# Optimization experiments

Measured on AMD Instinct MI355X. Metric: run time of the kernel, lower is better.

Reference implementation:

```python
import jax, jax.numpy as jnp
import numpy as np

I_SIZE = 8      # interval_size
WS = 8          # window_size
SHIFT = 4       # window_size // 2
HG = 4          # grid-attn heads (num_heads // 2)
HS = 4          # swin/window heads (num_heads // 2)


def cln(x, g, b, eps=1e-5):
    # channel LayerNorm over axis 1 of NCHW
    mu = x.mean(axis=1, keepdims=True)
    var = ((x - mu) ** 2).mean(axis=1, keepdims=True)
    return (x - mu) / jnp.sqrt(var + eps) * g[None, :, None, None] + b[None, :, None, None]


def conv1x1(x, w, b):
    return jnp.einsum('bchw,oc->bohw', x, w) + b[None, :, None, None]


def grid_shuffle(x, I):
    B, C, H, W = x.shape
    H1, W1 = H // I, W // I
    x = x.reshape(B, C, H1, I, W1, I).transpose(0, 3, 5, 1, 2, 4)
    return x.reshape(B * I * I, C, H1, W1)


def grid_unshuffle(x, I):
    Bi, C, H1, W1 = x.shape
    B = Bi // (I * I)
    x = x.reshape(B, I, I, C, H1, W1).transpose(0, 3, 4, 1, 5, 2)
    return x.reshape(B, C, H1 * I, W1 * I)


def rel_pos_index(wh, ww):
    coords = np.stack(np.meshgrid(np.arange(wh), np.arange(ww), indexing='ij')).reshape(2, -1)
    rel = (coords[:, :, None] - coords[:, None, :]).transpose(1, 2, 0)
    rel[:, :, 0] += wh - 1
    rel[:, :, 1] += ww - 1
    rel[:, :, 0] *= 2 * ww - 1
    return rel.sum(-1)  # (N, N) int


def dyn_pos_bias(H1, W1, w1, b1, w2, b2, w3, b3):
    # dynamic position bias MLP: (2,) relative coords -> heads
    ch = np.arange(1 - H1, H1, dtype=np.float32)
    cw = np.arange(1 - W1, W1, dtype=np.float32)
    rel = np.stack(np.meshgrid(ch, cw, indexing='ij'), axis=-1).reshape(-1, 2)
    t = jnp.asarray(rel)
    t = jax.nn.relu(t @ w1.T + b1)
    t = jax.nn.relu(t @ w2.T + b2)
    t = t @ w3.T + b3  # ((2H1-1)*(2W1-1), heads)
    idx = rel_pos_index(H1, W1)
    return t[idx].transpose(2, 0, 1)[None]  # (1, heads, N, N)


def mha2d(q, k, v, bias, heads, pw, pb):
    B, C, H, W = q.shape
    hd, N = C // heads, H * W
    sp = lambda t: t.reshape(B, heads, hd, N).transpose(0, 1, 3, 2)
    qh, kh, vh = sp(q), sp(k), sp(v)
    attn = jax.nn.softmax(jnp.einsum('bhnd,bhmd->bhnm', qh * hd ** -0.5, kh) + bias, axis=-1)
    out = jnp.einsum('bhnm,bhmd->bhnd', attn, vh).transpose(0, 1, 3, 2).reshape(B, C, H, W)
    return conv1x1(out, pw, pb)


def swin_mask(H, W, ws, shift):
    img = np.zeros((H, W), np.float32)
    cnt = 0
    for hs in (slice(0, H - ws), slice(H - ws, H - shift), slice(H - shift, H)):
        for wsl in (slice(0, W - ws), slice(W - ws, W - shift), slice(W - shift, W)):
            img[hs, wsl] = cnt
            cnt += 1
    mw = img.reshape(H // ws, ws, W // ws, ws).transpose(0, 2, 1, 3).reshape(-1, ws * ws)
    m = mw[:, None, :] - mw[:, :, None]
    return jnp.asarray(np.where(m != 0, -100.0, 0.0).astype(np.float32))  # (nW, N, N)


def swin_attn(x, qkv_w, qkv_b, rpb, pw, pb, ws, shift, heads):
    B, C, H, W = x.shape
    hd, N = C // heads, ws * ws
    if shift > 0:
        x = jnp.roll(x, (-shift, -shift), axis=(2, 3))
    nh, nw = H // ws, W // ws
    nW = nh * nw
    xw = x.reshape(B, C, nh, ws, nw, ws).transpose(0, 2, 4, 3, 5, 1).reshape(B * nW, N, C)
    qkv = (xw @ qkv_w.T + qkv_b).reshape(B * nW, N, 3, heads, hd).transpose(2, 0, 3, 1, 4)
    q, k, v = qkv[0], qkv[1], qkv[2]
    attn = jnp.einsum('bhnd,bhmd->bhnm', q * hd ** -0.5, k)
    attn = attn + rpb[rel_pos_index(ws, ws)].transpose(2, 0, 1)[None]
    if shift > 0:
        mask = swin_mask(H, W, ws, shift)
        attn = (attn.reshape(B, nW, heads, N, N) + mask[None, :, None]).reshape(B * nW, heads, N, N)
    attn = jax.nn.softmax(attn, axis=-1)
    out = jnp.einsum('bhnm,bhmd->bhnd', attn, v).transpose(0, 2, 1, 3).reshape(B * nW, N, C)
    out = out @ pw.T + pb
    out = out.reshape(B, nh, nw, ws, ws, C).transpose(0, 5, 1, 3, 2, 4).reshape(B, C, H, W)
    if shift > 0:
        out = jnp.roll(out, (shift, shift), axis=(2, 3))
    return out


def setup_inputs() -> dict:
    ks = iter(jax.random.split(jax.random.key(0), 64))
    w = lambda *s: jax.random.normal(next(ks), s, jnp.float32) * 0.02
    d, dg, ds, hid = 128, 64, 32, 256
    return dict(
        x=jax.random.normal(next(ks), (4, d, 128, 128), jnp.float32),
        ln_g=jnp.ones(d), ln_b=jnp.zeros(d),
        ga_qkv_w=w(3 * dg, dg), ga_qkv_b=jnp.zeros(3 * dg),
        ga_gp_w=w(dg, dg), ga_gp_b=jnp.zeros(dg),
        pos_w1=w(16, 2), pos_b1=jnp.zeros(16),
        pos_w2=w(16, 16), pos_b2=jnp.zeros(16),
        pos_w3=w(HG, 16), pos_b3=jnp.zeros(HG),
        a1_pw=w(dg, dg), a1_pb=jnp.zeros(dg),
        a2_pw=w(dg, dg), a2_pb=jnp.zeros(dg),
        sw_qkv_w=w(3 * ds, ds), sw_qkv_b=jnp.zeros(3 * ds),
        sw_rpb=w((2 * WS - 1) ** 2, HS), sw_pw=w(ds, ds), sw_pb=jnp.zeros(ds),
        wn_qkv_w=w(3 * ds, ds), wn_qkv_b=jnp.zeros(3 * ds),
        wn_rpb=w((2 * WS - 1) ** 2, HS), wn_pw=w(ds, ds), wn_pb=jnp.zeros(ds),
        fc_w=w(d, d), fc_b=jnp.zeros(d),
        n2_g=jnp.ones(d), n2_b=jnp.zeros(d),
        m1_w=w(hid, d), m1_b=jnp.zeros(hid),
        m2_w=w(d, hid), m2_b=jnp.zeros(d),
    )


def reference(x, ln_g, ln_b, ga_qkv_w, ga_qkv_b, ga_gp_w, ga_gp_b,
              pos_w1, pos_b1, pos_w2, pos_b2, pos_w3, pos_b3,
              a1_pw, a1_pb, a2_pw, a2_pb,
              sw_qkv_w, sw_qkv_b, sw_rpb, sw_pw, sw_pb,
              wn_qkv_w, wn_qkv_b, wn_rpb, wn_pw, wn_pb,
              fc_w, fc_b, n2_g, n2_b, m1_w, m1_b, m2_w, m2_b):
    B, C, H, W = x.shape
    shortcut = x
    xg, xs, xw = jnp.split(x, [C // 2, C // 2 + C // 4], axis=1)

    # --- grid attention branch (C/2 channels) ---
    qkv = conv1x1(xg, ga_qkv_w, ga_qkv_b)
    x_grid = conv1x1(grid_shuffle(xg, I_SIZE), ga_gp_w, ga_gp_b)
    qkv = grid_shuffle(qkv, I_SIZE)
    H1, W1 = H // I_SIZE, W // I_SIZE
    pbias = dyn_pos_bias(H1, W1, pos_w1, pos_b1, pos_w2, pos_b2, pos_w3, pos_b3)
    q, k, v = jnp.split(qkv, 3, axis=1)
    t = mha2d(x_grid, k, v, pbias, HG, a1_pw, a1_pb)
    t = mha2d(q, x_grid, t, pbias, HG, a2_pw, a2_pb)
    xg_attn = grid_unshuffle(t, I_SIZE)

    # --- shifted / plain window attention branches (C/4 each) ---
    xs_attn = swin_attn(xs, sw_qkv_w, sw_qkv_b, sw_rpb, sw_pw, sw_pb, WS, SHIFT, HS)
    xw_attn = swin_attn(xw, wn_qkv_w, wn_qkv_b, wn_rpb, wn_pw, wn_pb, WS, 0, HS)

    x = jnp.concatenate([xw_attn, xs_attn, xg_attn], axis=1)
    x = cln(conv1x1(x, fc_w, fc_b), ln_g, ln_b)
    x = shortcut + x
    h = conv1x1(x, m1_w, m1_b)
    h = jax.nn.gelu(h, approximate=False)
    h = conv1x1(h, m2_w, m2_b)
    return x + cln(h, n2_g, n2_b) + shortcut
```

## Files before the change

### kernel.cpp

```cpp
#include <hip/hip_runtime.h>
#include <hip/hip_bf16.h>
#include <cstdint>


typedef __attribute__((ext_vector_type(8))) short bf8_t;
typedef __attribute__((ext_vector_type(4))) float f4_t;

__device__ __forceinline__ float bf2f(unsigned short u) {
  union { unsigned int i; float f; } x; x.i = ((unsigned int)u) << 16; return x.f;
}
__device__ __forceinline__ unsigned short f2bf(float f) {
  union { float f; unsigned int i; } x; x.f = f;
  unsigned int r = x.i + 0x7FFFu + ((x.i >> 16) & 1u);
  return (unsigned short)(r >> 16);
}
__device__ __forceinline__ unsigned int pk2(float a, float b) {
  unsigned int d;
  asm("v_cvt_pk_bf16_f32 %0, %1, %2" : "=v"(d) : "v"(a), "v"(b));
  return d;
}

#define MB (1048576L)

__global__ void pos_mlp_k(const float* __restrict__ w1, const float* __restrict__ b1,
                          const float* __restrict__ w2, const float* __restrict__ b2,
                          const float* __restrict__ w3, const float* __restrict__ b3,
                          float* __restrict__ table) {
  int j = blockIdx.x * 256 + threadIdx.x;
  if (j >= 961) return;
  float chv = (float)(j / 31) - 15.0f;
  float cwv = (float)(j % 31) - 15.0f;
  float t1[16], t2[16];
#pragma unroll
  for (int i = 0; i < 16; ++i) {
    float s = fmaf(w1[i * 2], chv, fmaf(w1[i * 2 + 1], cwv, b1[i]));
    t1[i] = fmaxf(s, 0.0f);
  }
#pragma unroll
  for (int i = 0; i < 16; ++i) {
    float s = b2[i];
#pragma unroll
    for (int k = 0; k < 16; ++k) s = fmaf(w2[i * 16 + k], t1[k], s);
    t2[i] = fmaxf(s, 0.0f);
  }
#pragma unroll
  for (int hh = 0; hh < 4; ++hh) {
    float s = b3[hh];
#pragma unroll
    for (int k = 0; k < 16; ++k) s = fmaf(w3[hh * 16 + k], t2[k], s);
    table[j * 4 + hh] = s;
  }
}

__global__ void pbT_gather_k(const float* __restrict__ table, float* __restrict__ pbT) {
  int t = blockIdx.x * 256 + threadIdx.x;
  int hh = t >> 16;
  int r = t & 65535;
  int m = r >> 8;
  int q = r & 255;
  int idx = ((q >> 4) - (m >> 4) + 15) * 31 + ((q & 15) - (m & 15) + 15);
  pbT[t] = table[idx * 4 + hh];
}

__global__ void rpbT_k(const float* __restrict__ rpb, float* __restrict__ rpbT) {
  int t = blockIdx.x * 256 + threadIdx.x;
  int h = t >> 12, r = t & 4095, m = r >> 6, n = r & 63;
  int idx = ((n >> 3) - (m >> 3) + 7) * 15 + ((n & 7) - (m & 7) + 7);
  rpbT[t] = rpb[idx * 4 + h];
}

__global__ void wq2_k(const float* __restrict__ sw_w, const float* __restrict__ sw_b,
                      const float* __restrict__ wn_w, const float* __restrict__ wn_b,
                      unsigned short* __restrict__ w2, float* __restrict__ b2) {
  const float QS = 0.35355339059327373f;
  int t = blockIdx.x * 256 + threadIdx.x;
  if (t < 12288) {
    int row = t >> 6, col = t & 63;
    float v = 0.0f;
    if (row < 96) { if (col < 32) v = sw_w[row * 32 + col]; }
    else          { if (col >= 32) v = wn_w[(row - 96) * 32 + col - 32]; }
    int rb = row % 96;
    if (rb < 32) v *= QS;
    w2[t] = f2bf(v);
  }
  if (t < 192) {
    float v = t < 96 ? sw_b[t] : wn_b[t - 96];
    if ((t % 96) < 32) v *= QS;
    b2[t] = v;
  }
}

__global__ void wcvt_k(const float* __restrict__ w0, const float* __restrict__ w1,
                       const float* __restrict__ w2, const float* __restrict__ w3,
                       const float* __restrict__ w4, const float* __restrict__ w5,
                       const float* __restrict__ w6,
                       const float* __restrict__ qkv_b, const float* __restrict__ gp_b,
                       unsigned short* __restrict__ dst, float* __restrict__ biasQG) {
  int t = blockIdx.x * 256 + threadIdx.x;
  if (t < 256) biasQG[t] = t < 192 ? qkv_b[t] : gp_b[t - 192] * 0.25f;
  if (t >= 106496) return;
  const float* src; int off; float sc = 1.0f;
  if (t < 12288)      { src = w0; off = 0; }
  else if (t < 16384) { src = w1; off = 12288; sc = 0.25f; }
  else if (t < 20480) { src = w2; off = 16384; }
  else if (t < 24576) { src = w3; off = 20480; }
  else if (t < 40960) { src = w4; off = 24576; }
  else if (t < 73728) { src = w5; off = 40960; }
  else                { src = w6; off = 73728; }
  dst[t] = f2bf(src[t - off] * sc);
}

__global__ __launch_bounds__(256) void tin_k(const float* __restrict__ x,
                                             unsigned short* __restrict__ xTb) {
  __shared__ float tile[64][132];
  const int b = blockIdx.z, px0 = blockIdx.x * 64, tid = threadIdx.x;
#pragma unroll
  for (int i = 0; i < 8; ++i) {
    int e = i * 256 + tid;
    int c = e >> 4, p4 = (e & 15) * 4;
    float4 v = *(const float4*)(x + (((size_t)(b * 128 + c)) << 14) + px0 + p4);
    tile[p4][c] = v.x; tile[p4 + 1][c] = v.y; tile[p4 + 2][c] = v.z; tile[p4 + 3][c] = v.w;
  }
  __syncthreads();
#pragma unroll
  for (int i = 0; i < 8; ++i) {
    int e = i * 256 + tid;
    int px = e >> 5, c4 = (e & 31) * 4;
    uint2 w = {pk2(tile[px][c4], tile[px][c4 + 1]), pk2(tile[px][c4 + 2], tile[px][c4 + 3])};
    *(uint2*)(xTb + ((size_t)(b * 16384 + px0 + px)) * 128 + c4) = w;
  }
}

template <int NF, int KC, int EPI, int OSHUF>
__global__ __launch_bounds__(256) void gemm_k(
    const unsigned short* __restrict__ A, int a_rs, int a_c0,
    const unsigned short* __restrict__ W, const float* __restrict__ bias,
    const float* __restrict__ g, const float* __restrict__ bb,
    const unsigned short* __restrict__ resf, const unsigned short* __restrict__ resb,
    void* __restrict__ out, int o_rs, int o_c0) {
  __shared__ __align__(16) char Asw[128 * 128];
  __shared__ __align__(16) char Bsw[NF * 16 * 128];
  const int tid = threadIdx.x;
  const int lane = tid & 63, wv = tid >> 6, wpx = wv * 32;
  const int lr = lane & 15, lg = lane >> 4;
  const int px0 = blockIdx.x * 128;
  const int co0 = blockIdx.y * (NF * 16);

  f4_t acc[2][NF];
#pragma unroll
  for (int mf = 0; mf < 2; ++mf)
#pragma unroll
    for (int nf = 0; nf < NF; ++nf) acc[mf][nf] = (f4_t){0.f, 0.f, 0.f, 0.f};

  for (int kc = 0; kc < KC; ++kc) {
    const int k0 = kc * 64;
    if (kc) __syncthreads();
#pragma unroll
    for (int i = 0; i < 4; ++i) {
      int e = i * 256 + tid;
      int row = e >> 3, q8 = e & 7;
      const unsigned short* src = A + (size_t)(px0 + row) * a_rs + a_c0 + k0 + q8 * 8;
      *(uint4*)(Asw + row * 128 + ((q8 ^ (row & 7)) << 4)) = *(const uint4*)src;
    }
#pragma unroll
    for (int i = 0; i < NF / 2; ++i) {
      int e = i * 256 + tid;
      int row = e >> 3, q8 = e & 7;
      const unsigned short* src = W + (size_t)(co0 + row) * (KC * 64) + k0 + q8 * 8;
      *(uint4*)(Bsw + row * 128 + ((q8 ^ (row & 7)) << 4)) = *(const uint4*)src;
    }
    __syncthreads();
#pragma unroll
    for (int ks = 0; ks < 2; ++ks) {
      const int xk = (((ks * 4) + lg) ^ (lane & 7)) << 4;
      bf8_t av[2], bv[NF];
#pragma unroll
      for (int mf = 0; mf < 2; ++mf)
        av[mf] = *(const bf8_t*)(Asw + (wpx + mf * 16 + lr) * 128 + xk);
#pragma unroll
      for (int nf = 0; nf < NF; ++nf)
        bv[nf] = *(const bf8_t*)(Bsw + (nf * 16 + lr) * 128 + xk);
#pragma unroll
      for (int mf = 0; mf < 2; ++mf)
#pragma unroll
        for (int nf = 0; nf < NF; ++nf)
          acc[mf][nf] = __builtin_amdgcn_mfma_f32_16x16x32_bf16(av[mf], bv[nf], acc[mf][nf], 0, 0, 0);
    }
  }

  float bco[NF];
#pragma unroll
  for (int nf = 0; nf < NF; ++nf) bco[nf] = bias[co0 + nf * 16 + lr];

  if constexpr (EPI >= 2) {
    float gv[NF], bbv[NF];
#pragma unroll
    for (int nf = 0; nf < NF; ++nf) { gv[nf] = g[nf * 16 + lr]; bbv[nf] = bb[nf * 16 + lr]; }
#pragma unroll
    for (int mf = 0; mf < 2; ++mf)
#pragma unroll
      for (int nf = 0; nf < NF; ++nf)
#pragma unroll
        for (int r = 0; r < 4; ++r) acc[mf][nf][r] += bco[nf];
#pragma unroll
    for (int mf = 0; mf < 2; ++mf) {
      float mus[4], rss[4];
#pragma unroll
      for (int r = 0; r < 4; ++r) {
        float s = 0.f, q = 0.f;
#pragma unroll
        for (int nf = 0; nf < NF; ++nf) {
          float v = acc[mf][nf][r];
          s += v; q += v * v;
        }
#pragma unroll
        for (int msk = 1; msk < 16; msk <<= 1) {
          s += __shfl_xor(s, msk);
          q += __shfl_xor(q, msk);
        }
        float mu = s * (1.0f / 128.0f);
        float var = q * (1.0f / 128.0f) - mu * mu;
        mus[r] = mu;
        rss[r] = rsqrtf(var + 1e-5f);
      }
      if constexpr (EPI == 2) {
#pragma unroll
        for (int r = 0; r < 4; ++r) {
          int px_e = px0 + wpx + mf * 16 + lg * 4 + r;
          const unsigned short* xr = resf + (size_t)px_e * 128 + lr;
          unsigned short* op = (unsigned short*)out + (size_t)px_e * o_rs + lr;
#pragma unroll
          for (int nf = 0; nf < NF; ++nf) {
            float v = (acc[mf][nf][r] - mus[r]) * rss[r] * gv[nf] + bbv[nf] + bf2f(xr[nf * 16]);
            op[nf * 16] = f2bf(v);
          }
        }
      } else {
        int pxb = px0 + wpx + mf * 16 + lg * 4;
        int b_ = pxb >> 14, p_ = pxb & 16383;
#pragma unroll
        for (int nf = 0; nf < NF; ++nf) {
          int ch = lr + nf * 16;
          float vr[4];
#pragma unroll
          for (int r = 0; r < 4; ++r) {
            float xv  = bf2f(resf[(size_t)(pxb + r) * 128 + ch]);
            float x2v = bf2f(resb[(size_t)(pxb + r) * 128 + ch]);
            vr[r] = (acc[mf][nf][r] - mus[r]) * rss[r] * gv[nf] + bbv[nf] + xv + x2v;
          }
          float4 v4 = {vr[0], vr[1], vr[2], vr[3]};
          *(float4*)((float*)out + (((size_t)(b_ * 128 + ch)) << 14) + p_) = v4;
        }
      }
    }
  } else {
#pragma unroll
    for (int mf = 0; mf < 2; ++mf) {
#pragma unroll
      for (int r = 0; r < 4; ++r) {
        int px_e = px0 + wpx + mf * 16 + lg * 4 + r;
        size_t orow;
        int cadj = co0;
        if constexpr (OSHUF == 0) {
          orow = (size_t)px_e;
        } else if constexpr (OSHUF == 1) {
          int b = px_e >> 14, p = px_e & 16383, hh = p >> 7, w_ = p & 127;
          orow = (size_t)(b * 64 + (hh & 7) * 8 + (w_ & 7)) * 256 + ((hh >> 3) * 16 + (w_ >> 3));
        } else if constexpr (OSHUF == 2) {
          int gbb = px_e >> 8, n = px_e & 255;
          int b = gbb >> 6, ih = (gbb >> 3) & 7, iw = gbb & 7;
          orow = (size_t)b * 16384 + ((n >> 4) * 8 + ih) * 128 + (n & 15) * 8 + iw;
        } else {
          int brx = (co0 >= 96);
          int b = px_e >> 14, p = px_e & 16383, hh = p >> 7, w_ = p & 127;
          int sh = brx ? 0 : 4;
          int h2 = (hh - sh) & 127, w2_ = (w_ - sh) & 127;
          orow = (size_t)brx * 65536 + (size_t)b * 16384 +
                 (size_t)(((h2 >> 3) * 16 + (w2_ >> 3)) * 64 + (h2 & 7) * 8 + (w2_ & 7));
          cadj = co0 - brx * 96;
        }
        unsigned short* op = (unsigned short*)out + orow * o_rs + o_c0 + cadj + lr;
#pragma unroll
        for (int nf = 0; nf < NF; ++nf) {
          float v = acc[mf][nf][r] + bco[nf];
          if constexpr (EPI == 1) v = 0.5f * v * (1.0f + erff(v * 0.7071067811865475f));
          op[nf * 16] = f2bf(v);
        }
      }
    }
  }
}

__global__ __launch_bounds__(256) void gattn_k(
    const unsigned short* __restrict__ Q, int q_rs, int q_c0,
    const unsigned short* __restrict__ K, int k_rs, int k_c0,
    const unsigned short* __restrict__ V, int v_rs, int v_c0,
    const float* __restrict__ pbT, unsigned short* __restrict__ outb, int o_rs, int o_c0) {
  __shared__ __align__(16) unsigned short K_lds[256 * 16];
  __shared__ __align__(16) unsigned short Vt[16 * 256];
  __shared__ __align__(16) unsigned short P_lds[4 * 64 * 32];
  const int gb = blockIdx.x, h = blockIdx.y, tid = threadIdx.x;
  const int lane = tid & 63, wv = tid >> 6;
  const int lr = lane & 15, lg = lane >> 4;
  const int q0 = wv * 64;

  {
    const unsigned short* kp = K + (size_t)(gb * 256 + tid) * k_rs + k_c0 + h * 16;
    *(uint4*)&K_lds[tid * 16]     = *(const uint4*)kp;
    *(uint4*)&K_lds[tid * 16 + 8] = *(const uint4*)(kp + 8);
    const unsigned short* vp = V + (size_t)(gb * 256 + tid) * v_rs + v_c0 + h * 16;
    uint4 va = *(const uint4*)vp;
    uint4 vb = *(const uint4*)(vp + 8);
    unsigned int w8[8] = {va.x, va.y, va.z, va.w, vb.x, vb.y, vb.z, vb.w};
    int chb = (tid >> 3);
    int wi = tid & 7;
#pragma unroll
    for (int w = 0; w < 8; ++w) {
      int d0 = 2 * w, d1 = 2 * w + 1;
      Vt[d0 * 256 + ((chb ^ (d0 & 7)) << 3) + wi] = (unsigned short)(w8[w] & 0xffff);
      Vt[d1 * 256 + ((chb ^ (d1 & 7)) << 3) + wi] = (unsigned short)(w8[w] >> 16);
    }
  }
  bf8_t bq[4];
  const bf8_t bz = {0, 0, 0, 0, 0, 0, 0, 0};
#pragma unroll
  for (int qt = 0; qt < 4; ++qt) {
    bq[qt] = bz;
    if (lg < 2)
      bq[qt] = *(const bf8_t*)(Q + (size_t)(gb * 256 + q0 + qt * 16 + lr) * q_rs + q_c0 + h * 16 + lg * 8);
  }
  __syncthreads();

  const f4_t z4 = {0.f, 0.f, 0.f, 0.f};
  f4_t oacc[4];
  float lrun[4];
#pragma unroll
  for (int qt = 0; qt < 4; ++qt) { oacc[qt] = z4; lrun[qt] = 0.0f; }

  unsigned short* Pw = &P_lds[wv * 64 * 32];

  for (int m0 = 0; m0 < 256; m0 += 32) {
    bf8_t ak0 = bz, ak1 = bz;
    if (lg < 2) {
      ak0 = *(const bf8_t*)&K_lds[(m0 + lr) * 16 + lg * 8];
      ak1 = *(const bf8_t*)&K_lds[(m0 + 16 + lr) * 16 + lg * 8];
    }
    bf8_t av = *(const bf8_t*)&Vt[lr * 256 + ((((m0 >> 3) + lg) ^ (lr & 7)) << 3)];

#pragma unroll
    for (int qt = 0; qt < 4; ++qt) {
      const float* bpm = pbT + ((size_t)(h * 256 + m0 + lg * 4) << 8) + q0 + qt * 16 + lr;
      f4_t c0v = {bpm[0], bpm[256], bpm[512], bpm[768]};
      f4_t c1v = {bpm[4096], bpm[4352], bpm[4608], bpm[4864]};
      f4_t st0 = __builtin_amdgcn_mfma_f32_16x16x32_bf16(ak0, bq[qt], c0v, 0, 0, 0);
      f4_t st1 = __builtin_amdgcn_mfma_f32_16x16x32_bf16(ak1, bq[qt], c1v, 0, 0, 0);
      float p0[4], p1[4], ls = 0.0f;
#pragma unroll
      for (int r = 0; r < 4; ++r) {
        p0[r] = __expf(st0[r]);
        p1[r] = __expf(st1[r]);
        ls += p0[r] + p1[r];
      }
      ls += __shfl_xor(ls, 16);
      ls += __shfl_xor(ls, 32);
      lrun[qt] += ls;
      int row = qt * 16 + lr;
      int rw3 = row & 3;
      uint2 w0 = {pk2(p0[0], p0[1]), pk2(p0[2], p0[3])};
      uint2 w1 = {pk2(p1[0], p1[1]), pk2(p1[2], p1[3])};
      *(uint2*)&Pw[row * 32 + ((((lg >> 1)) ^ rw3) << 3) + (lg & 1) * 4]     = w0;
      *(uint2*)&Pw[row * 32 + (((2 + (lg >> 1)) ^ rw3) << 3) + (lg & 1) * 4] = w1;
    }
#pragma unroll
    for (int qt = 0; qt < 4; ++qt) {
      int row = qt * 16 + lr;
      bf8_t bp = *(const bf8_t*)&Pw[row * 32 + ((lg ^ (row & 3)) << 3)];
      oacc[qt] = __builtin_amdgcn_mfma_f32_16x16x32_bf16(av, bp, oacc[qt], 0, 0, 0);
    }
  }

#pragma unroll
  for (int qt = 0; qt < 4; ++qt) {
    float inv = 1.0f / lrun[qt];
    uint2 o;
    o.x = pk2(oacc[qt][0] * inv, oacc[qt][1] * inv);
    o.y = pk2(oacc[qt][2] * inv, oacc[qt][3] * inv);
    unsigned short* op = outb + (size_t)(gb * 256 + q0 + qt * 16 + lr) * o_rs + o_c0 + h * 16 + lg * 4;
    *(uint2*)op = o;
  }
}

__global__ __launch_bounds__(256) void swat_k(
    const unsigned short* __restrict__ qkv2,
    const float* __restrict__ rpbT_sw, const float* __restrict__ rpbT_wn,
    const float* __restrict__ sw_pw, const float* __restrict__ sw_pb,
    const float* __restrict__ wn_pw, const float* __restrict__ wn_pb,
    unsigned short* __restrict__ yT) {
  __shared__ __align__(16) unsigned short Vt[4 * 8 * 64];
  __shared__ __align__(16) unsigned short Pt[4 * 64 * 64];
  __shared__ __align__(16) unsigned short aoT[4 * 64 * 32];
  const int tid = threadIdx.x, lane = tid & 63, wv = tid >> 6;
  const int lr = lane & 15, lg = lane >> 4;
  const int br = blockIdx.y;
  const int win = blockIdx.x * 4 + wv;
  const int b = win >> 8, wl = win & 255, wh = wl >> 4, ww = wl & 15;
  const float* rpbT = br ? rpbT_wn : rpbT_sw;
  const float* pw   = br ? wn_pw : sw_pw;
  const float* pb   = br ? wn_pb : sw_pb;
  const int shift = br ? 0 : 4;
  const int yc0 = br ? 0 : 32;
  const bool edge = (shift > 0) && (wh == 15 || ww == 15);

  const unsigned short* qw = qkv2 + (size_t)br * 65536 * 96 + (size_t)win * 64 * 96;
  const f4_t z4 = {0.f, 0.f, 0.f, 0.f};
  const bf8_t bz = {0, 0, 0, 0, 0, 0, 0, 0};
  unsigned short* Vw = &Vt[wv * 8 * 64];
  unsigned short* Pw = &Pt[wv * 64 * 64];
  unsigned short* aw_ = &aoT[wv * 64 * 32];

#pragma unroll 1
  for (int h = 0; h < 4; ++h) {
    {
      uint4 v = *(const uint4*)(qw + lane * 96 + 64 + h * 8);
      unsigned int w4[4] = {v.x, v.y, v.z, v.w};
      int chb = lane >> 3, wi = lane & 7;
#pragma unroll
      for (int j = 0; j < 4; ++j) {
        int d0 = 2 * j, d1 = 2 * j + 1;
        Vw[d0 * 64 + ((chb ^ (d0 & 7)) << 3) + wi] = (unsigned short)(w4[j] & 0xffff);
        Vw[d1 * 64 + ((chb ^ (d1 & 7)) << 3) + wi] = (unsigned short)(w4[j] >> 16);
      }
    }
    bf8_t bq[4];
#pragma unroll
    for (int nt = 0; nt < 4; ++nt) {
      bq[nt] = bz;
      if (lg == 0) bq[nt] = *(const bf8_t*)(qw + (nt * 16 + lr) * 96 + h * 8);
    }
    f4_t st[4][4];
#pragma unroll
    for (int mt = 0; mt < 4; ++mt) {
      bf8_t ak = bz;
      if (lg == 0) ak = *(const bf8_t*)(qw + (mt * 16 + lr) * 96 + 32 + h * 8);
#pragma unroll
      for (int nt = 0; nt < 4; ++nt) {
        const float* rp = rpbT + h * 4096 + (mt * 16 + lg * 4) * 64 + nt * 16 + lr;
        f4_t cb = {rp[0], rp[64], rp[128], rp[192]};
        st[mt][nt] = __builtin_amdgcn_mfma_f32_16x16x32_bf16(ak, bq[nt], cb, 0, 0, 0);
      }
    }
#pragma unroll
    for (int nt = 0; nt < 4; ++nt) {
      float sv[16];
#pragma unroll
      for (int mt = 0; mt < 4; ++mt)
#pragma unroll
        for (int r = 0; r < 4; ++r) sv[mt * 4 + r] = st[mt][nt][r];
      if (edge) {
        int n = nt * 16 + lr;
        int regn = ((wh < 15) ? 0 : (((n >> 3) < 4) ? 1 : 2)) * 3 +
                   ((ww < 15) ? 0 : (((n & 7) < 4) ? 1 : 2));
#pragma unroll
        for (int mt = 0; mt < 4; ++mt)
#pragma unroll
          for (int r = 0; r < 4; ++r) {
            int m = mt * 16 + lg * 4 + r;
            int regm = ((wh < 15) ? 0 : (((m >> 3) < 4) ? 1 : 2)) * 3 +
                       ((ww < 15) ? 0 : (((m & 7) < 4) ? 1 : 2));
            if (regm != regn) sv[mt * 4 + r] -= 100.0f;
          }
      }
      float l = 0.0f;
#pragma unroll
      for (int i = 0; i < 16; ++i) {
        sv[i] = __expf(sv[i]);
        l += sv[i];
      }
      l += __shfl_xor(l, 16);
      l += __shfl_xor(l, 32);
      float inv = 1.0f / l;
      int row = nt * 16 + lr, rw7 = lr & 7;
#pragma unroll
      for (int mt = 0; mt < 4; ++mt) {
        uint2 w = {pk2(sv[mt * 4] * inv, sv[mt * 4 + 1] * inv),
                   pk2(sv[mt * 4 + 2] * inv, sv[mt * 4 + 3] * inv)};
        *(uint2*)&Pw[row * 64 + (((2 * mt + (lg >> 1)) ^ rw7) << 3) + (lg & 1) * 4] = w;
      }
    }
    f4_t oa[4] = {z4, z4, z4, z4};
#pragma unroll
    for (int ks = 0; ks < 2; ++ks) {
      bf8_t av = bz;
      if (lr < 8) av = *(const bf8_t*)&Vw[lr * 64 + (((4 * ks + lg) ^ (lr & 7)) << 3)];
#pragma unroll
      for (int nt = 0; nt < 4; ++nt) {
        int row = nt * 16 + lr;
        bf8_t bp = *(const bf8_t*)&Pw[row * 64 + (((4 * ks + lg) ^ (lr & 7)) << 3)];
        oa[nt] = __builtin_amdgcn_mfma_f32_16x16x32_bf16(av, bp, oa[nt], 0, 0, 0);
      }
    }
    if (lg < 2) {
#pragma unroll
      for (int nt = 0; nt < 4; ++nt) {
        uint2 w = {pk2(oa[nt][0], oa[nt][1]), pk2(oa[nt][2], oa[nt][3])};
        int row = nt * 16 + lr;
        *(uint2*)&aw_[row * 32 + ((h ^ (lr & 3)) << 3) + lg * 4] = w;
      }
    }
  }

#pragma unroll
  for (int mt = 0; mt < 2; ++mt) {
    const float* wr = pw + (mt * 16 + lr) * 32 + lg * 8;
    float4 a0 = *(const float4*)wr, a1 = *(const float4*)(wr + 4);
    union { uint4 u; bf8_t v; } aw;
    aw.u.x = pk2(a0.x, a0.y); aw.u.y = pk2(a0.z, a0.w);
    aw.u.z = pk2(a1.x, a1.y); aw.u.w = pk2(a1.z, a1.w);
    float pb0 = pb[mt * 16 + lg * 4], pb1 = pb[mt * 16 + lg * 4 + 1];
    float pb2 = pb[mt * 16 + lg * 4 + 2], pb3 = pb[mt * 16 + lg * 4 + 3];
#pragma unroll
    for (int nt = 0; nt < 4; ++nt) {
      int row = nt * 16 + lr;
      bf8_t bo = *(const bf8_t*)&aw_[row * 32 + ((lg ^ (lr & 3)) << 3)];
      f4_t po = __builtin_amdgcn_mfma_f32_16x16x32_bf16(aw.v, bo, z4, 0, 0, 0);
      int n = nt * 16 + lr;
      int hdst = (wh * 8 + (n >> 3) + shift) & 127;
      int wdst = (ww * 8 + (n & 7) + shift) & 127;
      uint2 w = {pk2(po[0] + pb0, po[1] + pb1), pk2(po[2] + pb2, po[3] + pb3)};
      *(uint2*)(yT + ((size_t)(b * 16384 + hdst * 128 + wdst)) * 128 + yc0 + mt * 16 + lg * 4) = w;
    }
  }
}

extern "C" void kernel_launch(void* const* d_in, const int* in_sizes, int n_in,
                              void* d_out, int out_size, void* d_ws, size_t ws_size,
                              hipStream_t stream) {
  (void)in_sizes; (void)n_in; (void)out_size; (void)ws_size;
  const float* x        = (const float*)d_in[0];
  const float* ln_g     = (const float*)d_in[1];
  const float* ln_b     = (const float*)d_in[2];
  const float* ga_qkv_w = (const float*)d_in[3];
  const float* ga_qkv_b = (const float*)d_in[4];
  const float* ga_gp_w  = (const float*)d_in[5];
  const float* ga_gp_b  = (const float*)d_in[6];
  const float* pos_w1   = (const float*)d_in[7];
  const float* pos_b1   = (const float*)d_in[8];
  const float* pos_w2   = (const float*)d_in[9];
  const float* pos_b2   = (const float*)d_in[10];
  const float* pos_w3   = (const float*)d_in[11];
  const float* pos_b3   = (const float*)d_in[12];
  const float* a1_pw    = (const float*)d_in[13];
  const float* a1_pb    = (const float*)d_in[14];
  const float* a2_pw    = (const float*)d_in[15];
  const float* a2_pb    = (const float*)d_in[16];
  const float* sw_qkv_w = (const float*)d_in[17];
  const float* sw_qkv_b = (const float*)d_in[18];
  const float* sw_rpb   = (const float*)d_in[19];
  const float* sw_pw    = (const float*)d_in[20];
  const float* sw_pb    = (const float*)d_in[21];
  const float* wn_qkv_w = (const float*)d_in[22];
  const float* wn_qkv_b = (const float*)d_in[23];
  const float* wn_rpb   = (const float*)d_in[24];
  const float* wn_pw    = (const float*)d_in[25];
  const float* wn_pb    = (const float*)d_in[26];
  const float* fc_w     = (const float*)d_in[27];
  const float* fc_b     = (const float*)d_in[28];
  const float* n2_g     = (const float*)d_in[29];
  const float* n2_b     = (const float*)d_in[30];
  const float* m1_w     = (const float*)d_in[31];
  const float* m1_b     = (const float*)d_in[32];
  const float* m2_w     = (const float*)d_in[33];
  const float* m2_b     = (const float*)d_in[34];
  float* out = (float*)d_out;
  char* base = (char*)d_ws;

  unsigned short* xTb    = (unsigned short*)(base);
  unsigned short* qgT    = (unsigned short*)(base + 16 * MB);
  unsigned short* t1T    = (unsigned short*)(base + 48 * MB);
  unsigned short* t1pT   = (unsigned short*)(base + 56 * MB);
  unsigned short* yT     = (unsigned short*)(base + 64 * MB);
  unsigned short* x2T    = (unsigned short*)(base + 80 * MB);
  unsigned short* qkv2   = (unsigned short*)(base + 16 * MB);
  unsigned short* hT     = (unsigned short*)(base + 16 * MB);
  float*          pbT    = (float*)(base + 96 * MB);
  float*          ptab   = (float*)(base + 97 * MB);
  float*          rpbT_sw= (float*)(base + 97 * MB + 65536);
  float*          rpbT_wn= (float*)(base + 97 * MB + 131072);
  unsigned short* wq2bf  = (unsigned short*)(base + 97 * MB + 196608);
  float*          bias192= (float*)(base + 97 * MB + 229376);
  float*          biasQG = (float*)(base + 97 * MB + 230400);
  unsigned short* wbf    = (unsigned short*)(base + 97 * MB + 262144);

  pos_mlp_k<<<4, 256, 0, stream>>>(pos_w1, pos_b1, pos_w2, pos_b2, pos_w3, pos_b3, ptab);
  pbT_gather_k<<<1024, 256, 0, stream>>>(ptab, pbT);
  rpbT_k<<<64, 256, 0, stream>>>(sw_rpb, rpbT_sw);
  rpbT_k<<<64, 256, 0, stream>>>(wn_rpb, rpbT_wn);
  wq2_k<<<48, 256, 0, stream>>>(sw_qkv_w, sw_qkv_b, wn_qkv_w, wn_qkv_b, wq2bf, bias192);
  wcvt_k<<<416, 256, 0, stream>>>(ga_qkv_w, ga_gp_w, a1_pw, a2_pw, fc_w, m1_w, m2_w,
                                  ga_qkv_b, ga_gp_b, wbf, biasQG);

  tin_k<<<dim3(256, 1, 4), 256, 0, stream>>>(x, xTb);

  gemm_k<4, 1, 0, 1><<<dim3(512, 4, 1), 256, 0, stream>>>(
      xTb, 128, 0, wbf, biasQG, nullptr, nullptr, nullptr, nullptr, qgT, 256, 0);

  gattn_k<<<dim3(256, 4), 256, 0, stream>>>(
      qgT, 256, 192, qgT, 256, 64, qgT, 256, 128, pbT, t1T, 64, 0);
  gemm_k<4, 1, 0, 0><<<dim3(512, 1, 1), 256, 0, stream>>>(
      t1T, 64, 0, wbf + 16384, a1_pb, nullptr, nullptr, nullptr, nullptr, t1pT, 64, 0);

  gattn_k<<<dim3(256, 4), 256, 0, stream>>>(
      qgT, 256, 0, qgT, 256, 192, t1pT, 64, 0, pbT, t1T, 64, 0);
  gemm_k<4, 1, 0, 2><<<dim3(512, 1, 1), 256, 0, stream>>>(
      t1T, 64, 0, wbf + 20480, a2_pb, nullptr, nullptr, nullptr, nullptr, yT, 128, 64);

  gemm_k<6, 1, 0, 3><<<dim3(512, 2, 1), 256, 0, stream>>>(
      xTb, 128, 64, wq2bf, bias192, nullptr, nullptr, nullptr, nullptr, qkv2, 96, 0);
  swat_k<<<dim3(256, 2), 256, 0, stream>>>(
      qkv2, rpbT_sw, rpbT_wn, sw_pw, sw_pb, wn_pw, wn_pb, yT);

  gemm_k<8, 2, 2, 0><<<dim3(512, 1, 1), 256, 0, stream>>>(
      yT, 128, 0, wbf + 24576, fc_b, ln_g, ln_b, xTb, nullptr, x2T, 128, 0);

  gemm_k<8, 2, 1, 0><<<dim3(512, 2, 1), 256, 0, stream>>>(
      x2T, 128, 0, wbf + 40960, m1_b, nullptr, nullptr, nullptr, nullptr, hT, 256, 0);
  gemm_k<8, 4, 3, 0><<<dim3(512, 1, 1), 256, 0, stream>>>(
      hT, 256, 0, wbf + 73728, m2_b, n2_g, n2_b, xTb, x2T, out, 128, 0);
}
```

Baseline: 194.6 us.

## Fuse MLP GEMMs into one kernel, merge setup kernels, store pos bias as bf16

Replaces the two MLP GEMM launches with a single mlp_k that keeps the GELU hidden activations for a 64-pixel tile in LDS, so the 256-channel hidden tensor is never written to or read from global memory. Merges the six weight and bias preparation kernels into one setup kernel, which cuts launch count. Stores the grid-attention position bias as bf16 laid out q-major, so gattn reads it with vector loads at half the bytes. The trade-offs are lower bias precision, larger LDS use per block, and W1 fragments read straight from global memory in the fused kernel.

```diff
diff --git a/kernel.cpp b/kernel.cpp
--- a/kernel.cpp
+++ b/kernel.cpp
@@ -22,92 +22,93 @@
 
 #define MB (1048576L)
 
-__global__ void pos_mlp_k(const float* __restrict__ w1, const float* __restrict__ b1,
-                          const float* __restrict__ w2, const float* __restrict__ b2,
-                          const float* __restrict__ w3, const float* __restrict__ b3,
-                          float* __restrict__ table) {
-  int j = blockIdx.x * 256 + threadIdx.x;
-  if (j >= 961) return;
-  float chv = (float)(j / 31) - 15.0f;
-  float cwv = (float)(j % 31) - 15.0f;
-  float t1[16], t2[16];
-#pragma unroll
-  for (int i = 0; i < 16; ++i) {
-    float s = fmaf(w1[i * 2], chv, fmaf(w1[i * 2 + 1], cwv, b1[i]));
-    t1[i] = fmaxf(s, 0.0f);
-  }
-#pragma unroll
-  for (int i = 0; i < 16; ++i) {
-    float s = b2[i];
-#pragma unroll
-    for (int k = 0; k < 16; ++k) s = fmaf(w2[i * 16 + k], t1[k], s);
-    t2[i] = fmaxf(s, 0.0f);
-  }
-#pragma unroll
-  for (int hh = 0; hh < 4; ++hh) {
-    float s = b3[hh];
-#pragma unroll
-    for (int k = 0; k < 16; ++k) s = fmaf(w3[hh * 16 + k], t2[k], s);
-    table[j * 4 + hh] = s;
-  }
-}
-
-__global__ void pbT_gather_k(const float* __restrict__ table, float* __restrict__ pbT) {
-  int t = blockIdx.x * 256 + threadIdx.x;
-  int hh = t >> 16;
-  int r = t & 65535;
-  int m = r >> 8;
-  int q = r & 255;
-  int idx = ((q >> 4) - (m >> 4) + 15) * 31 + ((q & 15) - (m & 15) + 15);
-  pbT[t] = table[idx * 4 + hh];
-}
-
-__global__ void rpbT_k(const float* __restrict__ rpb, float* __restrict__ rpbT) {
-  int t = blockIdx.x * 256 + threadIdx.x;
-  int h = t >> 12, r = t & 4095, m = r >> 6, n = r & 63;
-  int idx = ((n >> 3) - (m >> 3) + 7) * 15 + ((n & 7) - (m & 7) + 7);
-  rpbT[t] = rpb[idx * 4 + h];
-}
-
-__global__ void wq2_k(const float* __restrict__ sw_w, const float* __restrict__ sw_b,
-                      const float* __restrict__ wn_w, const float* __restrict__ wn_b,
-                      unsigned short* __restrict__ w2, float* __restrict__ b2) {
+__global__ void setup_k(
+    const float* __restrict__ w0, const float* __restrict__ w1,
+    const float* __restrict__ w2, const float* __restrict__ w3,
+    const float* __restrict__ w4, const float* __restrict__ w5,
+    const float* __restrict__ w6,
+    const float* __restrict__ qkv_b, const float* __restrict__ gp_b,
+    const float* __restrict__ sw_w, const float* __restrict__ sw_b,
+    const float* __restrict__ wn_w, const float* __restrict__ wn_b,
+    const float* __restrict__ sw_rpb, const float* __restrict__ wn_rpb,
+    const float* __restrict__ pw1, const float* __restrict__ pb1,
+    const float* __restrict__ pw2, const float* __restrict__ pb2,
+    const float* __restrict__ pw3, const float* __restrict__ pb3,
+    unsigned short* __restrict__ wbf, float* __restrict__ biasQG,
+    unsigned short* __restrict__ wq2, float* __restrict__ b192,
+    float* __restrict__ rpbT_sw, float* __restrict__ rpbT_wn,
+    float* __restrict__ ptab) {
   const float QS = 0.35355339059327373f;
   int t = blockIdx.x * 256 + threadIdx.x;
-  if (t < 12288) {
-    int row = t >> 6, col = t & 63;
+  if (t < 106496) {
+    const float* src; int off; float sc = 1.0f;
+    if (t < 12288)      { src = w0; off = 0; }
+    else if (t < 16384) { src = w1; off = 12288; sc = 0.25f; }
+    else if (t < 20480) { src = w2; off = 16384; }
+    else if (t < 24576) { src = w3; off = 20480; }
+    else if (t < 40960) { src = w4; off = 24576; }
+    else if (t < 73728) { src = w5; off = 40960; }
+    else                { src = w6; off = 73728; }
+    wbf[t] = f2bf(src[t - off] * sc);
+  } else if (t < 106752) {
+    int i = t - 106496;
+    biasQG[i] = i < 192 ? qkv_b[i] : gp_b[i - 192] * 0.25f;
+  } else if (t < 119040) {
+    int i = t - 106752;
+    int row = i >> 6, col = i & 63;
     float v = 0.0f;
     if (row < 96) { if (col < 32) v = sw_w[row * 32 + col]; }
     else          { if (col >= 32) v = wn_w[(row - 96) * 32 + col - 32]; }
-    int rb = row % 96;
-    if (rb < 32) v *= QS;
-    w2[t] = f2bf(v);
-  }
-  if (t < 192) {
-    float v = t < 96 ? sw_b[t] : wn_b[t - 96];
-    if ((t % 96) < 32) v *= QS;
-    b2[t] = v;
-  }
-}
-
-__global__ void wcvt_k(const float* __restrict__ w0, const float* __restrict__ w1,
-                       const float* __restrict__ w2, const float* __restrict__ w3,
-                       const float* __restrict__ w4, const float* __restrict__ w5,
-                       const float* __restrict__ w6,
-                       const float* __restrict__ qkv_b, const float* __restrict__ gp_b,
-                       unsigned short* __restrict__ dst, float* __restrict__ biasQG) {
+    if ((row % 96) < 32) v *= QS;
+    wq2[i] = f2bf(v);
+  } else if (t < 119232) {
+    int i = t - 119040;
+    float v = i < 96 ? sw_b[i] : wn_b[i - 96];
+    if ((i % 96) < 32) v *= QS;
+    b192[i] = v;
+  } else if (t < 152000) {
+    int i = t - 119232;
+    const float* rpb = i < 16384 ? sw_rpb : wn_rpb;
+    float* dst = i < 16384 ? rpbT_sw : rpbT_wn;
+    int j = i & 16383;
+    int h = j >> 12, r = j & 4095, m = r >> 6, n = r & 63;
+    int idx = ((n >> 3) - (m >> 3) + 7) * 15 + ((n & 7) - (m & 7) + 7);
+    dst[j] = rpb[idx * 4 + h];
+  } else if (t < 152961) {
+    int j = t - 152000;
+    float chv = (float)(j / 31) - 15.0f;
+    float cwv = (float)(j % 31) - 15.0f;
+    float t1[16], t2[16];
+#pragma unroll
+    for (int i = 0; i < 16; ++i) {
+      float s = fmaf(pw1[i * 2], chv, fmaf(pw1[i * 2 + 1], cwv, pb1[i]));
+      t1[i] = fmaxf(s, 0.0f);
+    }
+#pragma unroll
+    for (int i = 0; i < 16; ++i) {
+      float s = pb2[i];
+#pragma unroll
+      for (int k = 0; k < 16; ++k) s = fmaf(pw2[i * 16 + k], t1[k], s);
+      t2[i] = fmaxf(s, 0.0f);
+    }
+#pragma unroll
+    for (int hh = 0; hh < 4; ++hh) {
+      float s = pb3[hh];
+#pragma unroll
+      for (int k = 0; k < 16; ++k) s = fmaf(pw3[hh * 16 + k], t2[k], s);
+      ptab[j * 4 + hh] = s;
+    }
+  }
+}
+
+__global__ void pbq_k(const float* __restrict__ table, unsigned short* __restrict__ pbTq) {
   int t = blockIdx.x * 256 + threadIdx.x;
-  if (t < 256) biasQG[t] = t < 192 ? qkv_b[t] : gp_b[t - 192] * 0.25f;
-  if (t >= 106496) return;
-  const float* src; int off; float sc = 1.0f;
-  if (t < 12288)      { src = w0; off = 0; }
-  else if (t < 16384) { src = w1; off = 12288; sc = 0.25f; }
-  else if (t < 20480) { src = w2; off = 16384; }
-  else if (t < 24576) { src = w3; off = 20480; }
-  else if (t < 40960) { src = w4; off = 24576; }
-  else if (t < 73728) { src = w5; off = 40960; }
-  else                { src = w6; off = 73728; }
-  dst[t] = f2bf(src[t - off] * sc);
+  int h = t >> 16;
+  int r = t & 65535;
+  int q = r >> 8;
+  int m = r & 255;
+  int idx = ((q >> 4) - (m >> 4) + 15) * 31 + ((q & 15) - (m & 15) + 15);
+  pbTq[t] = f2bf(table[idx * 4 + h]);
 }
 
 __global__ __launch_bounds__(256) void tin_k(const float* __restrict__ x,
@@ -136,7 +137,7 @@
     const unsigned short* __restrict__ A, int a_rs, int a_c0,
     const unsigned short* __restrict__ W, const float* __restrict__ bias,
     const float* __restrict__ g, const float* __restrict__ bb,
-    const unsigned short* __restrict__ resf, const unsigned short* __restrict__ resb,
+    const unsigned short* __restrict__ resf,
     void* __restrict__ out, int o_rs, int o_c0) {
   __shared__ __align__(16) char Asw[128 * 128];
   __shared__ __align__(16) char Bsw[NF * 16 * 128];
@@ -192,7 +193,7 @@
 #pragma unroll
   for (int nf = 0; nf < NF; ++nf) bco[nf] = bias[co0 + nf * 16 + lr];
 
-  if constexpr (EPI >= 2) {
+  if constexpr (EPI == 2) {
     float gv[NF], bbv[NF];
 #pragma unroll
     for (int nf = 0; nf < NF; ++nf) { gv[nf] = g[nf * 16 + lr]; bbv[nf] = bb[nf * 16 + lr]; }
@@ -223,33 +224,15 @@
         mus[r] = mu;
         rss[r] = rsqrtf(var + 1e-5f);
       }
-      if constexpr (EPI == 2) {
-#pragma unroll
-        for (int r = 0; r < 4; ++r) {
-          int px_e = px0 + wpx + mf * 16 + lg * 4 + r;
-          const unsigned short* xr = resf + (size_t)px_e * 128 + lr;
-          unsigned short* op = (unsigned short*)out + (size_t)px_e * o_rs + lr;
-#pragma unroll
-          for (int nf = 0; nf < NF; ++nf) {
-            float v = (acc[mf][nf][r] - mus[r]) * rss[r] * gv[nf] + bbv[nf] + bf2f(xr[nf * 16]);
-            op[nf * 16] = f2bf(v);
-          }
-        }
-      } else {
-        int pxb = px0 + wpx + mf * 16 + lg * 4;
-        int b_ = pxb >> 14, p_ = pxb & 16383;
+#pragma unroll
+      for (int r = 0; r < 4; ++r) {
+        int px_e = px0 + wpx + mf * 16 + lg * 4 + r;
+        const unsigned short* xr = resf + (size_t)px_e * 128 + lr;
+        unsigned short* op = (unsigned short*)out + (size_t)px_e * o_rs + lr;
 #pragma unroll
         for (int nf = 0; nf < NF; ++nf) {
-          int ch = lr + nf * 16;
-          float vr[4];
-#pragma unroll
-          for (int r = 0; r < 4; ++r) {
-            float xv  = bf2f(resf[(size_t)(pxb + r) * 128 + ch]);
-            float x2v = bf2f(resb[(size_t)(pxb + r) * 128 + ch]);
-            vr[r] = (acc[mf][nf][r] - mus[r]) * rss[r] * gv[nf] + bbv[nf] + xv + x2v;
-          }
-          float4 v4 = {vr[0], vr[1], vr[2], vr[3]};
-          *(float4*)((float*)out + (((size_t)(b_ * 128 + ch)) << 14) + p_) = v4;
+          float v = (acc[mf][nf][r] - mus[r]) * rss[r] * gv[nf] + bbv[nf] + bf2f(xr[nf * 16]);
+          op[nf * 16] = f2bf(v);
         }
       }
     }
@@ -291,11 +274,147 @@
   }
 }
 
+__global__ __launch_bounds__(256) void mlp_k(
+    const unsigned short* __restrict__ x2T,
+    const unsigned short* __restrict__ W1, const float* __restrict__ b1,
+    const unsigned short* __restrict__ W2, const float* __restrict__ b2v,
+    const float* __restrict__ g, const float* __restrict__ bb,
+    const unsigned short* __restrict__ xTb,
+    float* __restrict__ out) {
+  __shared__ __align__(16) char SB[16384];
+  __shared__ __align__(16) unsigned short H[64 * 256];
+  const int tid = threadIdx.x, lane = tid & 63, wv = tid >> 6;
+  const int lr = lane & 15, lg = lane >> 4;
+  const int px0 = blockIdx.x * 64;
+  const f4_t z4 = {0.f, 0.f, 0.f, 0.f};
+
+  f4_t acc[4][4];
+#pragma unroll
+  for (int mf = 0; mf < 4; ++mf)
+#pragma unroll
+    for (int nf = 0; nf < 4; ++nf) acc[mf][nf] = z4;
+
+  for (int kc = 0; kc < 2; ++kc) {
+    if (kc) __syncthreads();
+#pragma unroll
+    for (int i = 0; i < 2; ++i) {
+      int e = i * 256 + tid;
+      int row = e >> 3, q8 = e & 7;
+      const unsigned short* src = x2T + (size_t)(px0 + row) * 128 + kc * 64 + q8 * 8;
+      *(uint4*)(SB + row * 128 + ((q8 ^ (row & 7)) << 4)) = *(const uint4*)src;
+    }
+    __syncthreads();
+#pragma unroll
+    for (int ks = 0; ks < 2; ++ks) {
+      const int xk = (((ks * 4) + lg) ^ (lane & 7)) << 4;
+      const int kof = kc * 64 + ks * 32 + lg * 8;
+      bf8_t av[4], bv[4];
+#pragma unroll
+      for (int mf = 0; mf < 4; ++mf)
+        av[mf] = *(const bf8_t*)(SB + (mf * 16 + lr) * 128 + xk);
+#pragma unroll
+      for (int nf = 0; nf < 4; ++nf)
+        bv[nf] = *(const bf8_t*)(W1 + (size_t)(wv * 64 + nf * 16 + lr) * 128 + kof);
+#pragma unroll
+      for (int mf = 0; mf < 4; ++mf)
+#pragma unroll
+        for (int nf = 0; nf < 4; ++nf)
+          acc[mf][nf] = __builtin_amdgcn_mfma_f32_16x16x32_bf16(av[mf], bv[nf], acc[mf][nf], 0, 0, 0);
+    }
+  }
+  __syncthreads();
+#pragma unroll
+  for (int nf = 0; nf < 4; ++nf) {
+    int ch = wv * 64 + nf * 16 + lr;
+    float bv = b1[ch];
+    int chunkbase = ch >> 3, cin = ch & 7;
+#pragma unroll
+    for (int mf = 0; mf < 4; ++mf) {
+#pragma unroll
+      for (int r = 0; r < 4; ++r) {
+        float v = acc[mf][nf][r] + bv;
+        v = 0.5f * v * (1.0f + erff(v * 0.7071067811865475f));
+        int px = mf * 16 + lg * 4 + r;
+        H[px * 256 + (((chunkbase ^ (px & 7)) << 3) + cin)] = f2bf(v);
+      }
+    }
+  }
+  __syncthreads();
+
+  f4_t a2[8];
+#pragma unroll
+  for (int nf = 0; nf < 8; ++nf) a2[nf] = z4;
+  const int pxl = wv * 16 + lr;
+  for (int kc = 0; kc < 4; ++kc) {
+    if (kc) __syncthreads();
+#pragma unroll
+    for (int i = 0; i < 4; ++i) {
+      int e = i * 256 + tid;
+      int row = e >> 3, q8 = e & 7;
+      const unsigned short* src = W2 + (size_t)row * 256 + kc * 64 + q8 * 8;
+      *(uint4*)(SB + row * 128 + ((q8 ^ (row & 7)) << 4)) = *(const uint4*)src;
+    }
+    __syncthreads();
+#pragma unroll
+    for (int ks = 0; ks < 2; ++ks) {
+      int chunk = ((kc * 8 + ks * 4 + lg) ^ (pxl & 7));
+      bf8_t av = *(const bf8_t*)&H[pxl * 256 + (chunk << 3)];
+      const int xk = (((ks * 4) + lg) ^ (lr & 7)) << 4;
+#pragma unroll
+      for (int nf = 0; nf < 8; ++nf) {
+        bf8_t bv = *(const bf8_t*)(SB + (nf * 16 + lr) * 128 + xk);
+        a2[nf] = __builtin_amdgcn_mfma_f32_16x16x32_bf16(av, bv, a2[nf], 0, 0, 0);
+      }
+    }
+  }
+  float gv[8], bbv[8];
+#pragma unroll
+  for (int nf = 0; nf < 8; ++nf) {
+    int ch = nf * 16 + lr;
+    gv[nf] = g[ch]; bbv[nf] = bb[ch];
+    float bc = b2v[ch];
+#pragma unroll
+    for (int r = 0; r < 4; ++r) a2[nf][r] += bc;
+  }
+  float mus[4], rss[4];
+#pragma unroll
+  for (int r = 0; r < 4; ++r) {
+    float s = 0.f, q = 0.f;
+#pragma unroll
+    for (int nf = 0; nf < 8; ++nf) { float v = a2[nf][r]; s += v; q += v * v; }
+#pragma unroll
+    for (int msk = 1; msk < 16; msk <<= 1) {
+      s += __shfl_xor(s, msk);
+      q += __shfl_xor(q, msk);
+    }
+    float mu = s * (1.0f / 128.0f);
+    float var = q * (1.0f / 128.0f) - mu * mu;
+    mus[r] = mu;
+    rss[r] = rsqrtf(var + 1e-5f);
+  }
+  int pxb = px0 + wv * 16 + lg * 4;
+  int b_ = pxb >> 14, p_ = pxb & 16383;
+#pragma unroll
+  for (int nf = 0; nf < 8; ++nf) {
+    int ch = nf * 16 + lr;
+    float vr[4];
+#pragma unroll
+    for (int r = 0; r < 4; ++r) {
+      float xv  = bf2f(xTb[(size_t)(pxb + r) * 128 + ch]);
+      float x2v = bf2f(x2T[(size_t)(pxb + r) * 128 + ch]);
+      vr[r] = (a2[nf][r] - mus[r]) * rss[r] * gv[nf] + bbv[nf] + xv + x2v;
+    }
+    float4 v4 = {vr[0], vr[1], vr[2], vr[3]};
+    *(float4*)(out + (((size_t)(b_ * 128 + ch)) << 14) + p_) = v4;
+  }
+}
+
 __global__ __launch_bounds__(256) void gattn_k(
     const unsigned short* __restrict__ Q, int q_rs, int q_c0,
     const unsigned short* __restrict__ K, int k_rs, int k_c0,
     const unsigned short* __restrict__ V, int v_rs, int v_c0,
-    const float* __restrict__ pbT, unsigned short* __restrict__ outb, int o_rs, int o_c0) {
+    const unsigned short* __restrict__ pbTq, unsigned short* __restrict__ outb,
+    int o_rs, int o_c0) {
   __shared__ __align__(16) unsigned short K_lds[256 * 16];
   __shared__ __align__(16) unsigned short Vt[16 * 256];
   __shared__ __align__(16) unsigned short P_lds[4 * 64 * 32];
@@ -349,9 +468,14 @@
 
 #pragma unroll
     for (int qt = 0; qt < 4; ++qt) {
-      const float* bpm = pbT + ((size_t)(h * 256 + m0 + lg * 4) << 8) + q0 + qt * 16 + lr;
-      f4_t c0v = {bpm[0], bpm[256], bpm[512], bpm[768]};
-      f4_t c1v = {bpm[4096], bpm[4352], bpm[4608], bpm[4864]};
+      const unsigned short* bq_ =
+          pbTq + (((size_t)(h * 256 + q0 + qt * 16 + lr)) << 8) + m0 + lg * 4;
+      uint2 u0 = *(const uint2*)bq_;
+      uint2 u1 = *(const uint2*)(bq_ + 16);
+      f4_t c0v = {bf2f((unsigned short)u0.x), bf2f((unsigned short)(u0.x >> 16)),
+                  bf2f((unsigned short)u0.y), bf2f((unsigned short)(u0.y >> 16))};
+      f4_t c1v = {bf2f((unsigned short)u1.x), bf2f((unsigned short)(u1.x >> 16)),
+                  bf2f((unsigned short)u1.y), bf2f((unsigned short)(u1.y >> 16))};
       f4_t st0 = __builtin_amdgcn_mfma_f32_16x16x32_bf16(ak0, bq[qt], c0v, 0, 0, 0);
       f4_t st1 = __builtin_amdgcn_mfma_f32_16x16x32_bf16(ak1, bq[qt], c1v, 0, 0, 0);
       float p0[4], p1[4], ls = 0.0f;
@@ -581,8 +705,7 @@
   unsigned short* yT     = (unsigned short*)(base + 64 * MB);
   unsigned short* x2T    = (unsigned short*)(base + 80 * MB);
   unsigned short* qkv2   = (unsigned short*)(base + 16 * MB);
-  unsigned short* hT     = (unsigned short*)(base + 16 * MB);
-  float*          pbT    = (float*)(base + 96 * MB);
+  unsigned short* pbTq   = (unsigned short*)(base + 96 * MB);
   float*          ptab   = (float*)(base + 97 * MB);
   float*          rpbT_sw= (float*)(base + 97 * MB + 65536);
   float*          rpbT_wn= (float*)(base + 97 * MB + 131072);
@@ -591,39 +714,38 @@
   float*          biasQG = (float*)(base + 97 * MB + 230400);
   unsigned short* wbf    = (unsigned short*)(base + 97 * MB + 262144);
 
-  pos_mlp_k<<<4, 256, 0, stream>>>(pos_w1, pos_b1, pos_w2, pos_b2, pos_w3, pos_b3, ptab);
-  pbT_gather_k<<<1024, 256, 0, stream>>>(ptab, pbT);
-  rpbT_k<<<64, 256, 0, stream>>>(sw_rpb, rpbT_sw);
-  rpbT_k<<<64, 256, 0, stream>>>(wn_rpb, rpbT_wn);
-  wq2_k<<<48, 256, 0, stream>>>(sw_qkv_w, sw_qkv_b, wn_qkv_w, wn_qkv_b, wq2bf, bias192);
-  wcvt_k<<<416, 256, 0, stream>>>(ga_qkv_w, ga_gp_w, a1_pw, a2_pw, fc_w, m1_w, m2_w,
-                                  ga_qkv_b, ga_gp_b, wbf, biasQG);
+  setup_k<<<598, 256, 0, stream>>>(
+      ga_qkv_w, ga_gp_w, a1_pw, a2_pw, fc_w, m1_w, m2_w,
+      ga_qkv_b, ga_gp_b,
+      sw_qkv_w, sw_qkv_b, wn_qkv_w, wn_qkv_b,
+      sw_rpb, wn_rpb,
+      pos_w1, pos_b1, pos_w2, pos_b2, pos_w3, pos_b3,
+      wbf, biasQG, wq2bf, bias192, rpbT_sw, rpbT_wn, ptab);
+  pbq_k<<<1024, 256, 0, stream>>>(ptab, pbTq);
 
   tin_k<<<dim3(256, 1, 4), 256, 0, stream>>>(x, xTb);
 
   gemm_k<4, 1, 0, 1><<<dim3(512, 4, 1), 256, 0, stream>>>(
-      xTb, 128, 0, wbf, biasQG, nullptr, nullptr, nullptr, nullptr, qgT, 256, 0);
+      xTb, 128, 0, wbf, biasQG, nullptr, nullptr, nullptr, qgT, 256, 0);
 
   gattn_k<<<dim3(256, 4), 256, 0, stream>>>(
-      qgT, 256, 192, qgT, 256, 64, qgT, 256, 128, pbT, t1T, 64, 0);
+      qgT, 256, 192, qgT, 256, 64, qgT, 256, 128, pbTq, t1T, 64, 0);
   gemm_k<4, 1, 0, 0><<<dim3(512, 1, 1), 256, 0, stream>>>(
-      t1T, 64, 0, wbf + 16384, a1_pb, nullptr, nullptr, nullptr, nullptr, t1pT, 64, 0);
+      t1T, 64, 0, wbf + 16384, a1_pb, nullptr, nullptr, nullptr, t1pT, 64, 0);
 
   gattn_k<<<dim3(256, 4), 256, 0, stream>>>(
-      qgT, 256, 0, qgT, 256, 192, t1pT, 64, 0, pbT, t1T, 64, 0);
+      qgT, 256, 0, qgT, 256, 192, t1pT, 64, 0, pbTq, t1T, 64, 0);
   gemm_k<4, 1, 0, 2><<<dim3(512, 1, 1), 256, 0, stream>>>(
-      t1T, 64, 0, wbf + 20480, a2_pb, nullptr, nullptr, nullptr, nullptr, yT, 128, 64);
+      t1T, 64, 0, wbf + 20480, a2_pb, nullptr, nullptr, nullptr, yT, 128, 64);
 
   gemm_k<6, 1, 0, 3><<<dim3(512, 2, 1), 256, 0, stream>>>(
-      xTb, 128, 64, wq2bf, bias192, nullptr, nullptr, nullptr, nullptr, qkv2, 96, 0);
+      xTb, 128, 64, wq2bf, bias192, nullptr, nullptr, nullptr, qkv2, 96, 0);
   swat_k<<<dim3(256, 2), 256, 0, stream>>>(
       qkv2, rpbT_sw, rpbT_wn, sw_pw, sw_pb, wn_pw, wn_pb, yT);
 
   gemm_k<8, 2, 2, 0><<<dim3(512, 1, 1), 256, 0, stream>>>(
-      yT, 128, 0, wbf + 24576, fc_b, ln_g, ln_b, xTb, nullptr, x2T, 128, 0);
-
-  gemm_k<8, 2, 1, 0><<<dim3(512, 2, 1), 256, 0, stream>>>(
-      x2T, 128, 0, wbf + 40960, m1_b, nullptr, nullptr, nullptr, nullptr, hT, 256, 0);
-  gemm_k<8, 4, 3, 0><<<dim3(512, 1, 1), 256, 0, stream>>>(
-      hT, 256, 0, wbf + 73728, m2_b, n2_g, n2_b, xTb, x2T, out, 128, 0);
-}
+      yT, 128, 0, wbf + 24576, fc_b, ln_g, ln_b, xTb, x2T, 128, 0);
+
+  mlp_k<<<1024, 256, 0, stream>>>(
+      x2T, wbf + 40960, m1_b, wbf + 73728, m2_b, n2_g, n2_b, xTb, out);
+}
```

Result: slower. 199.4 us (+2.5%).
